# Performance work log

Measured on AMD Instinct MI355X. Metric: run time of the kernel, lower is better.

Reference implementation:

```python
import jax, jax.numpy as jnp
import numpy as np

EMBED_DIM = 256
NUM_HEADS = 8
HEAD_DIM = EMBED_DIM // NUM_HEADS


def setup_inputs() -> dict:
    key = jax.random.key(0)
    ks = jax.random.split(key, 6)
    B, Nq, Nkv, C = 2, 4096, 4096, EMBED_DIM
    s = 0.02
    return {
        "query": jax.random.normal(ks[0], (B, Nq, C), dtype=jnp.float32),
        "key_value": jax.random.normal(ks[1], (B, Nkv, C), dtype=jnp.float32),
        "w_q": jax.random.normal(ks[2], (C, C), dtype=jnp.float32) * s,
        "w_kv": jax.random.normal(ks[3], (C, 2 * C), dtype=jnp.float32) * s,
        "w_out": jax.random.normal(ks[4], (C, C), dtype=jnp.float32) * s,
        "b_out": jax.random.normal(ks[5], (C,), dtype=jnp.float32) * s,
    }


def reference(query, key_value, w_q, w_kv, w_out, b_out):
    B, Nq, C = query.shape
    Nkv = key_value.shape[1]
    H, D = NUM_HEADS, HEAD_DIM
    scale = D ** -0.5
    # projections (Linear with no bias for q/kv)
    q = (query @ w_q).reshape(B, Nq, H, D).transpose(0, 2, 1, 3)       # [B,H,Nq,D]
    kv = (key_value @ w_kv).reshape(B, Nkv, 2, H, D)
    kv = kv.transpose(2, 0, 3, 1, 4)                                    # [2,B,H,Nkv,D]
    k, v = kv[0], kv[1]
    # full score matrix, as in the original (dropout = eval-mode identity)
    attn = jnp.einsum("bhqd,bhkd->bhqk", q, k) * scale                  # [B,H,Nq,Nkv]
    attn = jax.nn.softmax(attn, axis=-1)
    out = jnp.einsum("bhqk,bhkd->bhqd", attn, v)                        # [B,H,Nq,D]
    out = out.transpose(0, 2, 1, 3).reshape(B, Nq, C)
    return out @ w_out + b_out
```

## Files before the change

### kernel.cpp

```cpp
#include <hip/hip_runtime.h>

typedef __attribute__((ext_vector_type(8))) short bf16x8;
typedef __attribute__((ext_vector_type(4))) float f32x4;
typedef __attribute__((ext_vector_type(16))) float f32x16;

#define NQ   4096
#define NKV  4096
#define CDIM 256
#define HEADS 8
#define DDIM 32
#define APAD 264

__device__ __forceinline__ unsigned short f2bf(float x){
  unsigned int u = __builtin_bit_cast(unsigned int, x);
  u = (u + 0x7FFFu + ((u >> 16) & 1u)) >> 16;
  return (unsigned short)u;
}

__device__ __forceinline__ float bf2f_lo(unsigned int u){
  return __builtin_bit_cast(float, u << 16);
}
__device__ __forceinline__ float bf2f_hi(unsigned int u){
  return __builtin_bit_cast(float, u & 0xFFFF0000u);
}

__device__ __forceinline__ bf16x8 wfrag_f32(const float* __restrict__ w,
                                            int NW, int k, int n){
  const float* p = w + (size_t)k * NW + n;
  union { unsigned short u[8]; bf16x8 v; } o;
  #pragma unroll
  for (int j = 0; j < 8; ++j) o.u[j] = f2bf(p[(size_t)j * NW]);
  return o.v;
}

__global__ __launch_bounds__(256) void gemm_qkv3(
    const float* __restrict__ qf,
    const float* __restrict__ kvf,
    const float* __restrict__ wq,
    const float* __restrict__ wkv,
    unsigned short* __restrict__ QT,
    unsigned short* __restrict__ Kb,
    unsigned short* __restrict__ VTb)
{
  __shared__ unsigned short alds[64 * APAD];
  const int tid = threadIdx.x;
  const int wid = tid >> 6;
  const int lane = tid & 63;
  const int l15 = lane & 15, g = lane >> 4;
  const int m0 = blockIdx.x * 64;
  const int mode = blockIdx.y >= 4;
  const int ny = mode ? (blockIdx.y - 4) : blockIdx.y;
  const int n0 = ny * 64 + wid * 16;
  const float* Xf = mode ? kvf : qf;
  const float* W  = mode ? wkv : wq;
  const int NW    = mode ? 512 : 256;

  #pragma unroll
  for (int it = 0; it < 8; ++it){
    int c = it * 256 + tid;
    int row = c >> 5, col = (c & 31) * 8;
    const float4* src = (const float4*)(Xf + (size_t)(m0 + row) * CDIM + col);
    float4 a = src[0], b = src[1];
    union { unsigned short u[8]; bf16x8 v; } o;
    o.u[0]=f2bf(a.x); o.u[1]=f2bf(a.y); o.u[2]=f2bf(a.z); o.u[3]=f2bf(a.w);
    o.u[4]=f2bf(b.x); o.u[5]=f2bf(b.y); o.u[6]=f2bf(b.z); o.u[7]=f2bf(b.w);
    *(bf16x8*)(&alds[row * APAD + col]) = o.v;
  }
  __syncthreads();

  const int n = n0 + l15;
  f32x4 acc[4] = {{0,0,0,0},{0,0,0,0},{0,0,0,0},{0,0,0,0}};
  #pragma unroll
  for (int k0 = 0; k0 < CDIM; k0 += 32){
    bf16x8 bfr = wfrag_f32(W, NW, k0 + g*8, n);
    #pragma unroll
    for (int i = 0; i < 4; ++i){
      bf16x8 afr = *(const bf16x8*)(&alds[(l15 + i*16) * APAD + k0 + g*8]);
      acc[i] = __builtin_amdgcn_mfma_f32_16x16x32_bf16(afr, bfr, acc[i], 0, 0, 0);
    }
  }
  const int b = m0 >> 12;
  const int pos0b = (m0 & 4095) + g * 4;
  if (!mode){
    const int h = n >> 5, d = n & 31;
    const size_t rowbase = ((size_t)(b*HEADS + h)*DDIM + d) * NQ;
    #pragma unroll
    for (int i = 0; i < 4; ++i){
      unsigned int p0 = f2bf(acc[i][0] * 0.25503227f);
      unsigned int p1 = f2bf(acc[i][1] * 0.25503227f);
      unsigned int p2 = f2bf(acc[i][2] * 0.25503227f);
      unsigned int p3 = f2bf(acc[i][3] * 0.25503227f);
      *(uint2*)(&QT[rowbase + pos0b + i*16]) = make_uint2(p0 | (p1<<16), p2 | (p3<<16));
    }
  } else if (n < 256){
    const int h = n >> 5, d = n & 31;
    #pragma unroll
    for (int i = 0; i < 4; ++i){
      #pragma unroll
      for (int r = 0; r < 4; ++r){
        Kb[((size_t)(b*HEADS + h)*NKV + (pos0b + i*16 + r))*DDIM + d] = f2bf(acc[i][r]);
      }
    }
  } else {
    const int c = n - 256, h = c >> 5, d = c & 31;
    const size_t rowbase = ((size_t)(b*HEADS + h)*DDIM + d) * NKV;
    #pragma unroll
    for (int i = 0; i < 4; ++i){
      unsigned int p0 = f2bf(acc[i][0]);
      unsigned int p1 = f2bf(acc[i][1]);
      unsigned int p2 = f2bf(acc[i][2]);
      unsigned int p3 = f2bf(acc[i][3]);
      *(uint2*)(&VTb[rowbase + pos0b + i*16]) = make_uint2(p0 | (p1<<16), p2 | (p3<<16));
    }
  }
}

template<int NSPLIT>
__global__ __launch_bounds__(512, 4) void attn15(
    const unsigned short* __restrict__ QT,
    const unsigned short* __restrict__ Kb,
    const unsigned short* __restrict__ VT,
    unsigned short* __restrict__ P0, unsigned short* __restrict__ P1,
    unsigned short* __restrict__ P2, unsigned short* __restrict__ P3,
    float* __restrict__ ml)
{
  constexpr int NPHASE = 4096 / NSPLIT / 64;
  __shared__ unsigned short lk[4][2048];
  __shared__ unsigned short lv[4][2048];
  const int wid = threadIdx.x >> 6;
  const int lane = threadIdx.x & 63;
  const int l31 = lane & 31, g1 = lane >> 5;
  const int lin = blockIdx.x;
  const int xcd = lin & 7;
  const int j = lin >> 3;
  const int qg = j & 15;
  const int rest = j >> 4;
  const int kvpart = rest & (NSPLIT - 1);
  const int bh = xcd + 8 * (rest / NSPLIT);
  const int q0w = qg * 256 + wid * 32;
  const int kvoff = kvpart * (NPHASE * 64);

  const unsigned short* QTp = QT + (size_t)bh * DDIM * NQ;
  const unsigned short* KpH = Kb + ((size_t)bh * NKV + kvoff) * DDIM;
  const unsigned short* VpH = VT + (size_t)bh * DDIM * NKV + kvoff;

  union { unsigned short u[8]; bf16x8 v; } qa, qb;
  #pragma unroll
  for (int d = 0; d < 8; ++d)
    qa.u[d] = QTp[(size_t)(8*g1 + d) * NQ + q0w + l31];
  #pragma unroll
  for (int d = 0; d < 8; ++d)
    qb.u[d] = QTp[(size_t)(16 + 8*g1 + d) * NQ + q0w + l31];
  const bf16x8 qf0 = qa.v, qf1 = qb.v;

  union { unsigned short u[8]; bf16x8 v; } ones;
  #pragma unroll
  for (int jj = 0; jj < 8; ++jj) ones.u[jj] = 0x3F80;

  const unsigned short* gsrc;
  int gstep, cofs;
  unsigned short* larr;
  if (wid < 4){
    gsrc = KpH + (size_t)((wid >= 2 ? 32 : 0) + l31) * DDIM + 16*(wid & 1) + 8*g1;
    gstep = 64 * DDIM; larr = &lk[0][0]; cofs = wid * 512;
  } else {
    gsrc = VpH + (size_t)l31 * NKV + 16*(wid - 4) + 8*g1;
    gstep = 64; larr = &lv[0][0]; cofs = (wid - 4) * 512;
  }

  f32x16 acc, lac, zero16;
  #pragma unroll
  for (int jj = 0; jj < 16; ++jj){ acc[jj] = 0.0f; lac[jj] = 0.0f; zero16[jj] = 0.0f; }

  __builtin_amdgcn_global_load_lds((const unsigned int*)gsrc,
      (unsigned int*)(larr + cofs), 16, 0, 0);
  gsrc += gstep;
  __builtin_amdgcn_global_load_lds((const unsigned int*)gsrc,
      (unsigned int*)(larr + 2048 + cofs), 16, 0, 0);
  gsrc += gstep;

  int cur = 0, nxt = 2;
  for (int t = 0; t < NPHASE; ++t){
    const bool more = (t + 2) < NPHASE;
    const int dst = more ? nxt : 3;
    __builtin_amdgcn_global_load_lds((const unsigned int*)gsrc,
        (unsigned int*)(larr + dst * 2048 + cofs), 16, 0, 0);
    if (more) gsrc += gstep;
    __builtin_amdgcn_sched_barrier(0);
    asm volatile("s_waitcnt vmcnt(2)" ::: "memory");
    __builtin_amdgcn_s_barrier();
    __builtin_amdgcn_sched_barrier(0);

    bf16x8 kf0 = *(const bf16x8*)(&lk[cur][lane*8]);
    bf16x8 kf1 = *(const bf16x8*)(&lk[cur][512 + lane*8]);
    bf16x8 kf2 = *(const bf16x8*)(&lk[cur][1024 + lane*8]);
    bf16x8 kf3 = *(const bf16x8*)(&lk[cur][1536 + lane*8]);
    bf16x8 vf0 = *(const bf16x8*)(&lv[cur][lane*8]);
    bf16x8 vf1 = *(const bf16x8*)(&lv[cur][512 + lane*8]);
    bf16x8 vf2 = *(const bf16x8*)(&lv[cur][1024 + lane*8]);
    bf16x8 vf3 = *(const bf16x8*)(&lv[cur][1536 + lane*8]);

    __builtin_amdgcn_s_setprio(1);
    f32x16 sa = __builtin_amdgcn_mfma_f32_32x32x16_bf16(kf0, qf0, zero16, 0, 0, 0);
    sa = __builtin_amdgcn_mfma_f32_32x32x16_bf16(kf1, qf1, sa, 0, 0, 0);
    f32x16 sb = __builtin_amdgcn_mfma_f32_32x32x16_bf16(kf2, qf0, zero16, 0, 0, 0);
    sb = __builtin_amdgcn_mfma_f32_32x32x16_bf16(kf3, qf1, sb, 0, 0, 0);
    __builtin_amdgcn_s_setprio(0);

    #pragma unroll
    for (int jj = 0; jj < 16; ++jj) sa[jj] = __builtin_amdgcn_exp2f(sa[jj]);
    #pragma unroll
    for (int jj = 0; jj < 16; ++jj) sb[jj] = __builtin_amdgcn_exp2f(sb[jj]);

    unsigned int a0,a1,a2,a3,a4,a5,a6,a7, b0,b1,b2,b3,b4,b5,b6,b7;
    asm("v_cvt_pk_bf16_f32 %0, %1, %2" : "=v"(a0) : "v"(sa[0]),  "v"(sa[1]));
    asm("v_cvt_pk_bf16_f32 %0, %1, %2" : "=v"(a1) : "v"(sa[2]),  "v"(sa[3]));
    asm("v_cvt_pk_bf16_f32 %0, %1, %2" : "=v"(a2) : "v"(sa[4]),  "v"(sa[5]));
    asm("v_cvt_pk_bf16_f32 %0, %1, %2" : "=v"(a3) : "v"(sa[6]),  "v"(sa[7]));
    asm("v_cvt_pk_bf16_f32 %0, %1, %2" : "=v"(a4) : "v"(sa[8]),  "v"(sa[9]));
    asm("v_cvt_pk_bf16_f32 %0, %1, %2" : "=v"(a5) : "v"(sa[10]), "v"(sa[11]));
    asm("v_cvt_pk_bf16_f32 %0, %1, %2" : "=v"(a6) : "v"(sa[12]), "v"(sa[13]));
    asm("v_cvt_pk_bf16_f32 %0, %1, %2" : "=v"(a7) : "v"(sa[14]), "v"(sa[15]));
    asm("v_permlane32_swap_b32 %0, %1" : "+v"(a0), "+v"(a2));
    asm("v_permlane32_swap_b32 %0, %1" : "+v"(a1), "+v"(a3));
    asm("v_permlane32_swap_b32 %0, %1" : "+v"(a4), "+v"(a6));
    asm("v_permlane32_swap_b32 %0, %1" : "+v"(a5), "+v"(a7));
    asm("v_cvt_pk_bf16_f32 %0, %1, %2" : "=v"(b0) : "v"(sb[0]),  "v"(sb[1]));
    asm("v_cvt_pk_bf16_f32 %0, %1, %2" : "=v"(b1) : "v"(sb[2]),  "v"(sb[3]));
    asm("v_cvt_pk_bf16_f32 %0, %1, %2" : "=v"(b2) : "v"(sb[4]),  "v"(sb[5]));
    asm("v_cvt_pk_bf16_f32 %0, %1, %2" : "=v"(b3) : "v"(sb[6]),  "v"(sb[7]));
    asm("v_cvt_pk_bf16_f32 %0, %1, %2" : "=v"(b4) : "v"(sb[8]),  "v"(sb[9]));
    asm("v_cvt_pk_bf16_f32 %0, %1, %2" : "=v"(b5) : "v"(sb[10]), "v"(sb[11]));
    asm("v_cvt_pk_bf16_f32 %0, %1, %2" : "=v"(b6) : "v"(sb[12]), "v"(sb[13]));
    asm("v_cvt_pk_bf16_f32 %0, %1, %2" : "=v"(b7) : "v"(sb[14]), "v"(sb[15]));
    asm("v_permlane32_swap_b32 %0, %1" : "+v"(b0), "+v"(b2));
    asm("v_permlane32_swap_b32 %0, %1" : "+v"(b1), "+v"(b3));
    asm("v_permlane32_swap_b32 %0, %1" : "+v"(b4), "+v"(b6));
    asm("v_permlane32_swap_b32 %0, %1" : "+v"(b5), "+v"(b7));
    union { unsigned int u[4]; bf16x8 v; } fa0, fa1, fb0, fb1;
    fa0.u[0]=a0; fa0.u[1]=a1; fa0.u[2]=a2; fa0.u[3]=a3;
    fa1.u[0]=a4; fa1.u[1]=a5; fa1.u[2]=a6; fa1.u[3]=a7;
    fb0.u[0]=b0; fb0.u[1]=b1; fb0.u[2]=b2; fb0.u[3]=b3;
    fb1.u[0]=b4; fb1.u[1]=b5; fb1.u[2]=b6; fb1.u[3]=b7;

    __builtin_amdgcn_s_setprio(1);
    acc = __builtin_amdgcn_mfma_f32_32x32x16_bf16(vf0, fa0.v, acc, 0, 0, 0);
    acc = __builtin_amdgcn_mfma_f32_32x32x16_bf16(vf1, fa1.v, acc, 0, 0, 0);
    acc = __builtin_amdgcn_mfma_f32_32x32x16_bf16(vf2, fb0.v, acc, 0, 0, 0);
    acc = __builtin_amdgcn_mfma_f32_32x32x16_bf16(vf3, fb1.v, acc, 0, 0, 0);
    lac = __builtin_amdgcn_mfma_f32_32x32x16_bf16(ones.v, fa0.v, lac, 0, 0, 0);
    lac = __builtin_amdgcn_mfma_f32_32x32x16_bf16(ones.v, fa1.v, lac, 0, 0, 0);
    lac = __builtin_amdgcn_mfma_f32_32x32x16_bf16(ones.v, fb0.v, lac, 0, 0, 0);
    lac = __builtin_amdgcn_mfma_f32_32x32x16_bf16(ones.v, fb1.v, lac, 0, 0, 0);
    __builtin_amdgcn_s_setprio(0);

    cur = (cur == 2) ? 0 : cur + 1;
    nxt = (nxt == 2) ? 0 : nxt + 1;
  }

  float lsum = lac[0];
  unsigned short* Pp;
  if (NSPLIT == 2) Pp = kvpart ? P1 : P0;
  else { if (kvpart == 0) Pp = P0; else if (kvpart == 1) Pp = P1;
         else if (kvpart == 2) Pp = P2; else Pp = P3; }
  Pp += ((size_t)bh * NQ + q0w + l31) * DDIM;
  #pragma unroll
  for (int u = 0; u < 4; ++u){
    unsigned int w0, w1;
    asm("v_cvt_pk_bf16_f32 %0, %1, %2" : "=v"(w0) : "v"(acc[4*u+0]), "v"(acc[4*u+1]));
    asm("v_cvt_pk_bf16_f32 %0, %1, %2" : "=v"(w1) : "v"(acc[4*u+2]), "v"(acc[4*u+3]));
    *(uint2*)(Pp + 8*u + 4*g1) = make_uint2(w0, w1);
  }
  if (g1 == 0){
    size_t ridx = (size_t)bh * NQ + q0w + l31;
    ml[(size_t)kvpart * (16*NQ) + ridx] = lsum;
  }
}

template<int NP>
__global__ __launch_bounds__(512) void gemm_out3(
    const unsigned short* __restrict__ P0, const unsigned short* __restrict__ P1,
    const unsigned short* __restrict__ P2, const unsigned short* __restrict__ P3,
    const float* __restrict__ ml,
    const float* __restrict__ wout,
    float* __restrict__ FO,
    const float* __restrict__ bias)
{
  __shared__ unsigned short alds[32 * APAD];
  const int tid = threadIdx.x;
  const int m0 = blockIdx.x * 32;
  const int b = m0 >> 12;
  const int pos0 = m0 & 4095;
  const size_t R = (size_t)16 * NQ;
  const unsigned short* parr[4] = {P0, P1, P2, P3};

  #pragma unroll
  for (int it = 0; it < 2; ++it){
    int G = it * 512 + tid;
    int row = G >> 5, col8 = G & 31;
    int col = col8 * 8;
    int h = col8 >> 2, dcol = (col8 & 3) * 8;
    size_t ridx = (size_t)(b*HEADS + h) * NQ + pos0 + row;
    float lsum = 0.0f;
    #pragma unroll
    for (int p = 0; p < NP; ++p) lsum += ml[(size_t)p * R + ridx];
    float linv = 1.0f / lsum;
    float o[8] = {0,0,0,0,0,0,0,0};
    #pragma unroll
    for (int p = 0; p < NP; ++p){
      uint4 x = *(const uint4*)(parr[p] + ridx * DDIM + dcol);
      o[0] += bf2f_lo(x.x); o[1] += bf2f_hi(x.x);
      o[2] += bf2f_lo(x.y); o[3] += bf2f_hi(x.y);
      o[4] += bf2f_lo(x.z); o[5] += bf2f_hi(x.z);
      o[6] += bf2f_lo(x.w); o[7] += bf2f_hi(x.w);
    }
    unsigned int w[4];
    #pragma unroll
    for (int k = 0; k < 4; ++k){
      float a = o[2*k] * linv, bb = o[2*k+1] * linv;
      asm("v_cvt_pk_bf16_f32 %0, %1, %2" : "=v"(w[k]) : "v"(a), "v"(bb));
    }
    *(uint4*)(&alds[row * APAD + col]) = make_uint4(w[0], w[1], w[2], w[3]);
  }
  __syncthreads();

  const int wid = tid >> 6;
  const int lane = tid & 63;
  const int l15 = lane & 15, g = lane >> 4;
  const int n0 = wid * 32;
  f32x4 acc[2][2] = {{{0,0,0,0},{0,0,0,0}},{{0,0,0,0},{0,0,0,0}}};
  #pragma unroll
  for (int k0 = 0; k0 < CDIM; k0 += 32){
    bf16x8 bfr0 = wfrag_f32(wout, 256, k0 + g*8, n0 + l15);
    bf16x8 bfr1 = wfrag_f32(wout, 256, k0 + g*8, n0 + 16 + l15);
    bf16x8 afr0 = *(const bf16x8*)(&alds[(l15) * APAD + k0 + g*8]);
    bf16x8 afr1 = *(const bf16x8*)(&alds[(l15 + 16) * APAD + k0 + g*8]);
    acc[0][0] = __builtin_amdgcn_mfma_f32_16x16x32_bf16(afr0, bfr0, acc[0][0], 0, 0, 0);
    acc[0][1] = __builtin_amdgcn_mfma_f32_16x16x32_bf16(afr0, bfr1, acc[0][1], 0, 0, 0);
    acc[1][0] = __builtin_amdgcn_mfma_f32_16x16x32_bf16(afr1, bfr0, acc[1][0], 0, 0, 0);
    acc[1][1] = __builtin_amdgcn_mfma_f32_16x16x32_bf16(afr1, bfr1, acc[1][1], 0, 0, 0);
  }
  #pragma unroll
  for (int i = 0; i < 2; ++i){
    #pragma unroll
    for (int jj = 0; jj < 2; ++jj){
      int n = n0 + jj*16 + l15;
      float bv = bias[n];
      #pragma unroll
      for (int r = 0; r < 4; ++r){
        int m = m0 + i*16 + g*4 + r;
        FO[(size_t)m * CDIM + n] = acc[i][jj][r] + bv;
      }
    }
  }
}

extern "C" void kernel_launch(void* const* d_in, const int* in_sizes, int n_in,
                              void* d_out, int out_size, void* d_ws, size_t ws_size,
                              hipStream_t stream)
{
  const float* query     = (const float*)d_in[0];
  const float* key_value = (const float*)d_in[1];
  const float* w_q       = (const float*)d_in[2];
  const float* w_kv      = (const float*)d_in[3];
  const float* w_out     = (const float*)d_in[4];
  const float* b_out     = (const float*)d_in[5];
  float* out = (float*)d_out;
  char* ws = (char*)d_ws;
  unsigned short* P0    = (unsigned short*)(ws + 0);
  unsigned short* P1    = (unsigned short*)(ws + 4194304);
  unsigned short* QT    = (unsigned short*)(ws + 8912896);
  unsigned short* Kb    = (unsigned short*)(ws + 13107200);
  unsigned short* VTb   = (unsigned short*)(ws + 17301504);

  const int nsplit = (ws_size >= 30932992u) ? 4 : 2;
  unsigned short *P2, *P3;
  float* mlb;
  if (nsplit == 4){
    P2  = (unsigned short*)(ws + 21495808);
    P3  = (unsigned short*)(ws + 25690112);
    mlb = (float*)(ws + 29884416);
  } else {
    P2 = P0; P3 = P1;
    mlb = (float*)(ws + 21495808);
  }

  gemm_qkv3<<<dim3(128, 12), 256, 0, stream>>>(query, key_value, w_q, w_kv, QT, Kb, VTb);
  if (nsplit == 4){
    attn15<4><<<1024, 512, 0, stream>>>(QT, Kb, VTb, P0, P1, P2, P3, mlb);
    gemm_out3<4><<<256, 512, 0, stream>>>(P0, P1, P2, P3, mlb, w_out, out, b_out);
  } else {
    attn15<2><<<512, 512, 0, stream>>>(QT, Kb, VTb, P0, P1, P2, P3, mlb);
    gemm_out3<2><<<256, 512, 0, stream>>>(P0, P1, P2, P3, mlb, w_out, out, b_out);
  }
}
```

Before: 75.33 us.

## Software-pipeline attention loop: overlap PV of previous tile with QK of current

Restructures the attention inner loop so that each iteration issues the PV/rowsum MFMAs for the previous KV tile before the QK MFMAs and exp/convert of the current tile. The packed probabilities are carried across iterations in registers. The LDS ring grows from 4 to 5 buffers so the previous tile's V stays resident while new tiles stream in. The aim is to hide the exp/convert/permlane latency behind independent MFMA work, at the cost of more live registers and more LDS per block, which may reduce occupancy.

```diff
diff --git a/kernel.cpp b/kernel.cpp
--- a/kernel.cpp
+++ b/kernel.cpp
@@ -115,8 +115,86 @@
   }
 }
 
+#define QKSTEP20(CURB)                                                                 \
+  do {                                                                                 \
+    const unsigned short* bK = &lk[(CURB)][0];                                         \
+    bf16x8 kf0 = *(const bf16x8*)(bK + lane*8);                                        \
+    bf16x8 kf1 = *(const bf16x8*)(bK + 512 + lane*8);                                  \
+    bf16x8 kf2 = *(const bf16x8*)(bK + 1024 + lane*8);                                 \
+    bf16x8 kf3 = *(const bf16x8*)(bK + 1536 + lane*8);                                 \
+    __builtin_amdgcn_s_setprio(1);                                                     \
+    f32x16 sa = __builtin_amdgcn_mfma_f32_32x32x16_bf16(kf0, qf0, zero16, 0, 0, 0);    \
+    sa = __builtin_amdgcn_mfma_f32_32x32x16_bf16(kf1, qf1, sa, 0, 0, 0);               \
+    f32x16 sb = __builtin_amdgcn_mfma_f32_32x32x16_bf16(kf2, qf0, zero16, 0, 0, 0);    \
+    sb = __builtin_amdgcn_mfma_f32_32x32x16_bf16(kf3, qf1, sb, 0, 0, 0);               \
+    __builtin_amdgcn_s_setprio(0);                                                     \
+    _Pragma("unroll")                                                                  \
+    for (int jj = 0; jj < 16; ++jj) sa[jj] = __builtin_amdgcn_exp2f(sa[jj]);           \
+    _Pragma("unroll")                                                                  \
+    for (int jj = 0; jj < 16; ++jj) sb[jj] = __builtin_amdgcn_exp2f(sb[jj]);           \
+    asm("v_cvt_pk_bf16_f32 %0, %1, %2" : "=v"(pk0)  : "v"(sa[0]),  "v"(sa[1]));        \
+    asm("v_cvt_pk_bf16_f32 %0, %1, %2" : "=v"(pk1)  : "v"(sa[2]),  "v"(sa[3]));        \
+    asm("v_cvt_pk_bf16_f32 %0, %1, %2" : "=v"(pk2)  : "v"(sa[4]),  "v"(sa[5]));        \
+    asm("v_cvt_pk_bf16_f32 %0, %1, %2" : "=v"(pk3)  : "v"(sa[6]),  "v"(sa[7]));        \
+    asm("v_cvt_pk_bf16_f32 %0, %1, %2" : "=v"(pk4)  : "v"(sa[8]),  "v"(sa[9]));        \
+    asm("v_cvt_pk_bf16_f32 %0, %1, %2" : "=v"(pk5)  : "v"(sa[10]), "v"(sa[11]));       \
+    asm("v_cvt_pk_bf16_f32 %0, %1, %2" : "=v"(pk6)  : "v"(sa[12]), "v"(sa[13]));       \
+    asm("v_cvt_pk_bf16_f32 %0, %1, %2" : "=v"(pk7)  : "v"(sa[14]), "v"(sa[15]));       \
+    asm("v_permlane32_swap_b32 %0, %1" : "+v"(pk0), "+v"(pk2));                        \
+    asm("v_permlane32_swap_b32 %0, %1" : "+v"(pk1), "+v"(pk3));                        \
+    asm("v_permlane32_swap_b32 %0, %1" : "+v"(pk4), "+v"(pk6));                        \
+    asm("v_permlane32_swap_b32 %0, %1" : "+v"(pk5), "+v"(pk7));                        \
+    asm("v_cvt_pk_bf16_f32 %0, %1, %2" : "=v"(pk8)  : "v"(sb[0]),  "v"(sb[1]));        \
+    asm("v_cvt_pk_bf16_f32 %0, %1, %2" : "=v"(pk9)  : "v"(sb[2]),  "v"(sb[3]));        \
+    asm("v_cvt_pk_bf16_f32 %0, %1, %2" : "=v"(pk10) : "v"(sb[4]),  "v"(sb[5]));        \
+    asm("v_cvt_pk_bf16_f32 %0, %1, %2" : "=v"(pk11) : "v"(sb[6]),  "v"(sb[7]));        \
+    asm("v_cvt_pk_bf16_f32 %0, %1, %2" : "=v"(pk12) : "v"(sb[8]),  "v"(sb[9]));        \
+    asm("v_cvt_pk_bf16_f32 %0, %1, %2" : "=v"(pk13) : "v"(sb[10]), "v"(sb[11]));       \
+    asm("v_cvt_pk_bf16_f32 %0, %1, %2" : "=v"(pk14) : "v"(sb[12]), "v"(sb[13]));       \
+    asm("v_cvt_pk_bf16_f32 %0, %1, %2" : "=v"(pk15) : "v"(sb[14]), "v"(sb[15]));       \
+    asm("v_permlane32_swap_b32 %0, %1" : "+v"(pk8),  "+v"(pk10));                      \
+    asm("v_permlane32_swap_b32 %0, %1" : "+v"(pk9),  "+v"(pk11));                      \
+    asm("v_permlane32_swap_b32 %0, %1" : "+v"(pk12), "+v"(pk14));                      \
+    asm("v_permlane32_swap_b32 %0, %1" : "+v"(pk13), "+v"(pk15));                      \
+  } while (0)
+
+#define PVSTEP20(PRVB)                                                                 \
+  do {                                                                                 \
+    const unsigned short* bV = &lv[(PRVB)][0];                                         \
+    bf16x8 vf0 = *(const bf16x8*)(bV + lane*8);                                        \
+    bf16x8 vf1 = *(const bf16x8*)(bV + 512 + lane*8);                                  \
+    bf16x8 vf2 = *(const bf16x8*)(bV + 1024 + lane*8);                                 \
+    bf16x8 vf3 = *(const bf16x8*)(bV + 1536 + lane*8);                                 \
+    union { unsigned int u[4]; bf16x8 v; } fa0, fa1, fb0, fb1;                         \
+    fa0.u[0]=pk0;  fa0.u[1]=pk1;  fa0.u[2]=pk2;  fa0.u[3]=pk3;                         \
+    fa1.u[0]=pk4;  fa1.u[1]=pk5;  fa1.u[2]=pk6;  fa1.u[3]=pk7;                         \
+    fb0.u[0]=pk8;  fb0.u[1]=pk9;  fb0.u[2]=pk10; fb0.u[3]=pk11;                        \
+    fb1.u[0]=pk12; fb1.u[1]=pk13; fb1.u[2]=pk14; fb1.u[3]=pk15;                        \
+    __builtin_amdgcn_s_setprio(1);                                                     \
+    acc = __builtin_amdgcn_mfma_f32_32x32x16_bf16(vf0, fa0.v, acc, 0, 0, 0);           \
+    acc = __builtin_amdgcn_mfma_f32_32x32x16_bf16(vf1, fa1.v, acc, 0, 0, 0);           \
+    acc = __builtin_amdgcn_mfma_f32_32x32x16_bf16(vf2, fb0.v, acc, 0, 0, 0);           \
+    acc = __builtin_amdgcn_mfma_f32_32x32x16_bf16(vf3, fb1.v, acc, 0, 0, 0);           \
+    lac = __builtin_amdgcn_mfma_f32_32x32x16_bf16(ones.v, fa0.v, lac, 0, 0, 0);        \
+    lac = __builtin_amdgcn_mfma_f32_32x32x16_bf16(ones.v, fa1.v, lac, 0, 0, 0);        \
+    lac = __builtin_amdgcn_mfma_f32_32x32x16_bf16(ones.v, fb0.v, lac, 0, 0, 0);        \
+    lac = __builtin_amdgcn_mfma_f32_32x32x16_bf16(ones.v, fb1.v, lac, 0, 0, 0);        \
+    __builtin_amdgcn_s_setprio(0);                                                     \
+  } while (0)
+
+#define STAGE_SYNC20(DSTB, MORE)                                                       \
+  do {                                                                                 \
+    __builtin_amdgcn_global_load_lds((const unsigned int*)gsrc,                        \
+        (unsigned int*)(larr + (DSTB) * 2048 + cofs), 16, 0, 0);                       \
+    if (MORE) gsrc += gstep;                                                           \
+    __builtin_amdgcn_sched_barrier(0);                                                 \
+    asm volatile("s_waitcnt vmcnt(2)" ::: "memory");                                   \
+    __builtin_amdgcn_s_barrier();                                                      \
+    __builtin_amdgcn_sched_barrier(0);                                                 \
+  } while (0)
+
 template<int NSPLIT>
-__global__ __launch_bounds__(512, 4) void attn15(
+__global__ __launch_bounds__(512, 4) void attn20(
     const unsigned short* __restrict__ QT,
     const unsigned short* __restrict__ Kb,
     const unsigned short* __restrict__ VT,
@@ -125,8 +203,8 @@
     float* __restrict__ ml)
 {
   constexpr int NPHASE = 4096 / NSPLIT / 64;
-  __shared__ unsigned short lk[4][2048];
-  __shared__ unsigned short lv[4][2048];
+  __shared__ unsigned short lk[5][2048];
+  __shared__ unsigned short lv[5][2048];
   const int wid = threadIdx.x >> 6;
   const int lane = threadIdx.x & 63;
   const int l31 = lane & 31, g1 = lane >> 5;
@@ -171,6 +249,7 @@
   f32x16 acc, lac, zero16;
   #pragma unroll
   for (int jj = 0; jj < 16; ++jj){ acc[jj] = 0.0f; lac[jj] = 0.0f; zero16[jj] = 0.0f; }
+  unsigned int pk0,pk1,pk2,pk3,pk4,pk5,pk6,pk7,pk8,pk9,pk10,pk11,pk12,pk13,pk14,pk15;
 
   __builtin_amdgcn_global_load_lds((const unsigned int*)gsrc,
       (unsigned int*)(larr + cofs), 16, 0, 0);
@@ -179,84 +258,20 @@
       (unsigned int*)(larr + 2048 + cofs), 16, 0, 0);
   gsrc += gstep;
 
-  int cur = 0, nxt = 2;
-  for (int t = 0; t < NPHASE; ++t){
+  STAGE_SYNC20(2, true);
+  QKSTEP20(0);
+
+  int cur = 1, prv = 0, dst = 3;
+  for (int t = 1; t < NPHASE; ++t){
     const bool more = (t + 2) < NPHASE;
-    const int dst = more ? nxt : 3;
-    __builtin_amdgcn_global_load_lds((const unsigned int*)gsrc,
-        (unsigned int*)(larr + dst * 2048 + cofs), 16, 0, 0);
-    if (more) gsrc += gstep;
-    __builtin_amdgcn_sched_barrier(0);
-    asm volatile("s_waitcnt vmcnt(2)" ::: "memory");
-    __builtin_amdgcn_s_barrier();
-    __builtin_amdgcn_sched_barrier(0);
-
-    bf16x8 kf0 = *(const bf16x8*)(&lk[cur][lane*8]);
-    bf16x8 kf1 = *(const bf16x8*)(&lk[cur][512 + lane*8]);
-    bf16x8 kf2 = *(const bf16x8*)(&lk[cur][1024 + lane*8]);
-    bf16x8 kf3 = *(const bf16x8*)(&lk[cur][1536 + lane*8]);
-    bf16x8 vf0 = *(const bf16x8*)(&lv[cur][lane*8]);
-    bf16x8 vf1 = *(const bf16x8*)(&lv[cur][512 + lane*8]);
-    bf16x8 vf2 = *(const bf16x8*)(&lv[cur][1024 + lane*8]);
-    bf16x8 vf3 = *(const bf16x8*)(&lv[cur][1536 + lane*8]);
-
-    __builtin_amdgcn_s_setprio(1);
-    f32x16 sa = __builtin_amdgcn_mfma_f32_32x32x16_bf16(kf0, qf0, zero16, 0, 0, 0);
-    sa = __builtin_amdgcn_mfma_f32_32x32x16_bf16(kf1, qf1, sa, 0, 0, 0);
-    f32x16 sb = __builtin_amdgcn_mfma_f32_32x32x16_bf16(kf2, qf0, zero16, 0, 0, 0);
-    sb = __builtin_amdgcn_mfma_f32_32x32x16_bf16(kf3, qf1, sb, 0, 0, 0);
-    __builtin_amdgcn_s_setprio(0);
-
-    #pragma unroll
-    for (int jj = 0; jj < 16; ++jj) sa[jj] = __builtin_amdgcn_exp2f(sa[jj]);
-    #pragma unroll
-    for (int jj = 0; jj < 16; ++jj) sb[jj] = __builtin_amdgcn_exp2f(sb[jj]);
-
-    unsigned int a0,a1,a2,a3,a4,a5,a6,a7, b0,b1,b2,b3,b4,b5,b6,b7;
-    asm("v_cvt_pk_bf16_f32 %0, %1, %2" : "=v"(a0) : "v"(sa[0]),  "v"(sa[1]));
-    asm("v_cvt_pk_bf16_f32 %0, %1, %2" : "=v"(a1) : "v"(sa[2]),  "v"(sa[3]));
-    asm("v_cvt_pk_bf16_f32 %0, %1, %2" : "=v"(a2) : "v"(sa[4]),  "v"(sa[5]));
-    asm("v_cvt_pk_bf16_f32 %0, %1, %2" : "=v"(a3) : "v"(sa[6]),  "v"(sa[7]));
-    asm("v_cvt_pk_bf16_f32 %0, %1, %2" : "=v"(a4) : "v"(sa[8]),  "v"(sa[9]));
-    asm("v_cvt_pk_bf16_f32 %0, %1, %2" : "=v"(a5) : "v"(sa[10]), "v"(sa[11]));
-    asm("v_cvt_pk_bf16_f32 %0, %1, %2" : "=v"(a6) : "v"(sa[12]), "v"(sa[13]));
-    asm("v_cvt_pk_bf16_f32 %0, %1, %2" : "=v"(a7) : "v"(sa[14]), "v"(sa[15]));
-    asm("v_permlane32_swap_b32 %0, %1" : "+v"(a0), "+v"(a2));
-    asm("v_permlane32_swap_b32 %0, %1" : "+v"(a1), "+v"(a3));
-    asm("v_permlane32_swap_b32 %0, %1" : "+v"(a4), "+v"(a6));
-    asm("v_permlane32_swap_b32 %0, %1" : "+v"(a5), "+v"(a7));
-    asm("v_cvt_pk_bf16_f32 %0, %1, %2" : "=v"(b0) : "v"(sb[0]),  "v"(sb[1]));
-    asm("v_cvt_pk_bf16_f32 %0, %1, %2" : "=v"(b1) : "v"(sb[2]),  "v"(sb[3]));
-    asm("v_cvt_pk_bf16_f32 %0, %1, %2" : "=v"(b2) : "v"(sb[4]),  "v"(sb[5]));
-    asm("v_cvt_pk_bf16_f32 %0, %1, %2" : "=v"(b3) : "v"(sb[6]),  "v"(sb[7]));
-    asm("v_cvt_pk_bf16_f32 %0, %1, %2" : "=v"(b4) : "v"(sb[8]),  "v"(sb[9]));
-    asm("v_cvt_pk_bf16_f32 %0, %1, %2" : "=v"(b5) : "v"(sb[10]), "v"(sb[11]));
-    asm("v_cvt_pk_bf16_f32 %0, %1, %2" : "=v"(b6) : "v"(sb[12]), "v"(sb[13]));
-    asm("v_cvt_pk_bf16_f32 %0, %1, %2" : "=v"(b7) : "v"(sb[14]), "v"(sb[15]));
-    asm("v_permlane32_swap_b32 %0, %1" : "+v"(b0), "+v"(b2));
-    asm("v_permlane32_swap_b32 %0, %1" : "+v"(b1), "+v"(b3));
-    asm("v_permlane32_swap_b32 %0, %1" : "+v"(b4), "+v"(b6));
-    asm("v_permlane32_swap_b32 %0, %1" : "+v"(b5), "+v"(b7));
-    union { unsigned int u[4]; bf16x8 v; } fa0, fa1, fb0, fb1;
-    fa0.u[0]=a0; fa0.u[1]=a1; fa0.u[2]=a2; fa0.u[3]=a3;
-    fa1.u[0]=a4; fa1.u[1]=a5; fa1.u[2]=a6; fa1.u[3]=a7;
-    fb0.u[0]=b0; fb0.u[1]=b1; fb0.u[2]=b2; fb0.u[3]=b3;
-    fb1.u[0]=b4; fb1.u[1]=b5; fb1.u[2]=b6; fb1.u[3]=b7;
-
-    __builtin_amdgcn_s_setprio(1);
-    acc = __builtin_amdgcn_mfma_f32_32x32x16_bf16(vf0, fa0.v, acc, 0, 0, 0);
-    acc = __builtin_amdgcn_mfma_f32_32x32x16_bf16(vf1, fa1.v, acc, 0, 0, 0);
-    acc = __builtin_amdgcn_mfma_f32_32x32x16_bf16(vf2, fb0.v, acc, 0, 0, 0);
-    acc = __builtin_amdgcn_mfma_f32_32x32x16_bf16(vf3, fb1.v, acc, 0, 0, 0);
-    lac = __builtin_amdgcn_mfma_f32_32x32x16_bf16(ones.v, fa0.v, lac, 0, 0, 0);
-    lac = __builtin_amdgcn_mfma_f32_32x32x16_bf16(ones.v, fa1.v, lac, 0, 0, 0);
-    lac = __builtin_amdgcn_mfma_f32_32x32x16_bf16(ones.v, fb0.v, lac, 0, 0, 0);
-    lac = __builtin_amdgcn_mfma_f32_32x32x16_bf16(ones.v, fb1.v, lac, 0, 0, 0);
-    __builtin_amdgcn_s_setprio(0);
-
-    cur = (cur == 2) ? 0 : cur + 1;
-    nxt = (nxt == 2) ? 0 : nxt + 1;
-  }
+    STAGE_SYNC20(dst, more);
+    PVSTEP20(prv);
+    QKSTEP20(cur);
+    prv = cur;
+    cur = (cur == 4) ? 0 : cur + 1;
+    dst = (dst == 4) ? 0 : dst + 1;
+  }
+  PVSTEP20(prv);
 
   float lsum = lac[0];
   unsigned short* Pp;
@@ -387,10 +402,10 @@
 
   gemm_qkv3<<<dim3(128, 12), 256, 0, stream>>>(query, key_value, w_q, w_kv, QT, Kb, VTb);
   if (nsplit == 4){
-    attn15<4><<<1024, 512, 0, stream>>>(QT, Kb, VTb, P0, P1, P2, P3, mlb);
+    attn20<4><<<1024, 512, 0, stream>>>(QT, Kb, VTb, P0, P1, P2, P3, mlb);
     gemm_out3<4><<<256, 512, 0, stream>>>(P0, P1, P2, P3, mlb, w_out, out, b_out);
   } else {
-    attn15<2><<<512, 512, 0, stream>>>(QT, Kb, VTb, P0, P1, P2, P3, mlb);
+    attn20<2><<<512, 512, 0, stream>>>(QT, Kb, VTb, P0, P1, P2, P3, mlb);
     gemm_out3<2><<<256, 512, 0, stream>>>(P0, P1, P2, P3, mlb, w_out, out, b_out);
   }
 }
```

After: 75.92 us. Within noise of the previous version (+0.8%).
